# Kernel optimization log

Measured on AMD Instinct MI355X. Metric: run time of the kernel, lower is better.

The kernel has to match this reference:

```python
import jax, jax.numpy as jnp
import numpy as np


def _phi(x):
    # ELU(x) + 1 feature map (positive kernel feature map)
    return jax.nn.elu(x) + 1.0


def setup_inputs() -> dict:
    key = jax.random.key(0)
    k1, k2, k3 = jax.random.split(key, 3)
    B, S, E = 4, 4096, 1024
    inputs = jax.random.normal(k1, (B, S, E), dtype=jnp.float32)
    mask = jnp.ones((B, S), dtype=jnp.float32)
    w_qkv = jax.random.normal(k2, (3 * E, E), dtype=jnp.float32) * (E ** -0.5)
    b_qkv = jax.random.normal(k3, (3 * E,), dtype=jnp.float32) * 0.02
    return {"inputs": inputs, "mask": mask, "w_qkv": w_qkv, "b_qkv": b_qkv, "num_heads": 16}


def reference(inputs, mask, w_qkv, b_qkv, num_heads):
    B, S, E = inputs.shape
    H = num_heads
    D = E // H
    # qkv projection: torch Linear is x @ W.T + b
    qkv = inputs @ w_qkv.T + b_qkv                     # (B, S, 3E)
    qkv = qkv.reshape(B, S, 3, H, D)
    q = qkv[:, :, 0]                                   # (B, S, H, D)
    k = qkv[:, :, 1]
    v = qkv[:, :, 2]
    # key masking (float multiply, as in einsum 'bshd,bs->bshd')
    k = k * mask[:, :, None, None]
    kq = _phi(q)                                       # (B, S, H, D)
    kk = _phi(k)                                       # (B, S, H, D)
    # kv outer-product accumulation over sequence: (B, H, M, D)
    kv = jnp.einsum('bshd,bshm->bhmd', kk, v)
    # normalizer
    z = 1.0 / (jnp.einsum('bshd,bhd->bsh', kq, kk.sum(axis=1)) + 1e-6)
    # final contraction
    attn = jnp.einsum('bshd,bhmd,bsh->bshm', kq, kv, z)  # (B, S, H, D)
    attn = attn.reshape(B, S, E)
    # NOTE: original forward computes a projection but returns `attn` (dropout is
    # identity at inference), so projection is dead code and omitted here.
    return attn
```

## Files before the change

kernel.cpp:

```cpp
#include <hip/hip_runtime.h>

typedef unsigned short u16;
typedef short bf16x8 __attribute__((ext_vector_type(8)));
typedef float f32x4 __attribute__((ext_vector_type(4)));
typedef u16 u16x8 __attribute__((ext_vector_type(8)));
typedef u16 u16x4 __attribute__((ext_vector_type(4)));

#define B_ 4
#define S_ 4096
#define E_ 1024
#define H_ 16
#define D_ 64
#define M_ 16384
#define N_ 3072
#define K_ 1024

__device__ __forceinline__ u16 f2b(float f) {
    unsigned x = __builtin_bit_cast(unsigned, f);
    return (u16)((x + 0x7fffu + ((x >> 16) & 1u)) >> 16);
}
__device__ __forceinline__ float b2f(u16 u) {
    unsigned x = ((unsigned)u) << 16;
    return __builtin_bit_cast(float, x);
}
__device__ __forceinline__ float phi_f(float x) { return x > 0.f ? x + 1.f : __expf(x); }

__device__ __forceinline__ void gload16(const void* g, void* l) {
    __builtin_amdgcn_global_load_lds((const __attribute__((address_space(1))) void*)g,
                                     (__attribute__((address_space(3))) void*)l, 16, 0, 0);
}

#define MEMFENCE asm volatile("" ::: "memory")
#define BAR { MEMFENCE; __builtin_amdgcn_s_barrier(); MEMFENCE; }
#define LGKM0 { asm volatile("s_waitcnt lgkmcnt(0)" ::: "memory"); \
                __builtin_amdgcn_sched_barrier(0); }
#define VMCNT(n) asm volatile("s_waitcnt vmcnt(" #n ")" ::: "memory")

__global__ void cvt_bf16(const float* __restrict__ in, u16* __restrict__ out, int n8) {
    int stride = gridDim.x * blockDim.x;
    for (int i = blockIdx.x * blockDim.x + threadIdx.x; i < n8; i += stride) {
        const float4* p = (const float4*)(in + (size_t)i * 8);
        float4 a = p[0], b = p[1];
        u16x8 o;
        o[0] = f2b(a.x); o[1] = f2b(a.y); o[2] = f2b(a.z); o[3] = f2b(a.w);
        o[4] = f2b(b.x); o[5] = f2b(b.y); o[6] = f2b(b.z); o[7] = f2b(b.w);
        *(u16x8*)(out + (size_t)i * 8) = o;
    }
}


#define RD_A(BO, MI0) { _Pragma("unroll") for (int m_ = 0; m_ < 4; ++m_) { \
    av[m_][0] = *(const bf16x8*)(aB + (BO) + (MI0 + m_) * 2048 + pc0); \
    av[m_][1] = *(const bf16x8*)(aB + (BO) + (MI0 + m_) * 2048 + pc1); } }

#define RD_B01(BO) { _Pragma("unroll") for (int n_ = 0; n_ < 2; ++n_) { \
    b01[n_][0] = *(const bf16x8*)(bB + (BO) + n_ * 2048 + pc0); \
    b01[n_][1] = *(const bf16x8*)(bB + (BO) + n_ * 2048 + pc1); } }

#define RD_B23(BO) { _Pragma("unroll") for (int n_ = 0; n_ < 2; ++n_) { \
    b23[n_][0] = *(const bf16x8*)(bB + (BO) + (2 + n_) * 2048 + pc0); \
    b23[n_][1] = *(const bf16x8*)(bB + (BO) + (2 + n_) * 2048 + pc1); } }

#define ST_A(TT, HI, BO) { \
    gload16(gA + (size_t)((HI) * 64) * K_ + (TT) * 64, lds + (BO) + (HI) * 8192 + t16); \
    gload16(gA + (size_t)((HI) * 64 + 128) * K_ + (TT) * 64, lds + (BO) + 16384 + (HI) * 8192 + t16); }

#define ST_B(TT, PR, BO) { \
    gload16(gB + (size_t)((PR) * 128) * K_ + (TT) * 64, lds + (BO) + 32768 + (PR) * 16384 + t16); \
    gload16(gB + (size_t)((PR) * 128 + 64) * K_ + (TT) * 64, lds + (BO) + 32768 + (PR) * 16384 + 8192 + t16); }

#define MM16(MI0, NI0, BV) { __builtin_amdgcn_s_setprio(1); \
    _Pragma("unroll") for (int m_ = 0; m_ < 4; ++m_) \
    _Pragma("unroll") for (int n_ = 0; n_ < 2; ++n_) \
    _Pragma("unroll") for (int h_ = 0; h_ < 2; ++h_) \
        acc[(MI0) + m_][(NI0) + n_] = __builtin_amdgcn_mfma_f32_16x16x32_bf16( \
            av[m_][h_], BV[n_][h_], acc[(MI0) + m_][(NI0) + n_], 0, 0, 0); \
    __builtin_amdgcn_s_setprio(0); }

__device__ __forceinline__ void run_tile(
    const u16* gA, const u16* gB, char* lds, int t16,
    const char* aB, const char* bB, int pc0, int pc1, f32x4 (&acc)[8][4])
{
    bf16x8 av[4][2], b01[2][2], b23[2][2];
    ST_A(0, 0, 0); ST_B(0, 0, 0); ST_B(0, 1, 0); ST_A(0, 1, 0);
    ST_A(1, 0, 65536); ST_B(1, 0, 65536);
    VMCNT(4);
    __builtin_amdgcn_s_barrier();
    MEMFENCE;
#pragma unroll 1
    for (int kt = 0; kt < 16; kt += 2) {
        int tp2 = kt + 2 < 16 ? kt + 2 : 15;
        int tp3 = kt + 3 < 16 ? kt + 3 : 15;
        RD_A(0, 0); RD_B01(0); ST_A(kt + 1, 1, 65536); BAR; LGKM0; MM16(0, 0, b01);
        RD_B23(0);  ST_B(kt + 1, 1, 65536);            BAR; LGKM0; MM16(0, 2, b23);
        RD_A(0, 4); ST_A(tp2, 0, 0);                   BAR; LGKM0; MM16(4, 2, b23);
        ST_B(tp2, 0, 0); VMCNT(4);                     BAR; LGKM0; MM16(4, 0, b01);
        RD_A(65536, 0); RD_B01(65536); ST_A(tp2, 1, 0); BAR; LGKM0; MM16(0, 0, b01);
        RD_B23(65536);  ST_B(tp2, 1, 0);                BAR; LGKM0; MM16(0, 2, b23);
        RD_A(65536, 4); ST_A(tp3, 0, 65536);            BAR; LGKM0; MM16(4, 2, b23);
        ST_B(tp3, 0, 65536); VMCNT(4);                  BAR; LGKM0; MM16(4, 0, b01);
    }
    VMCNT(0);
    __builtin_amdgcn_s_barrier();
    MEMFENCE;
}

__global__ __launch_bounds__(512, 2) void gemm_vk(
    const u16* __restrict__ Abf, const u16* __restrict__ Wbf,
    const float* __restrict__ bias, const float* __restrict__ mask,
    u16* VT, float* __restrict__ KVP, float* __restrict__ KSP)
{
    __shared__ __align__(16) char lds[131072];

    int wg  = blockIdx.x;
    int xcd = wg & 7, ii = wg >> 3;
    int tm  = xcd * 8 + (ii >> 2);
    int g   = ii & 3;
    int m0  = tm << 8;
    int b   = tm >> 4;
    int s0  = (tm & 15) << 8;

    int t = threadIdx.x;
    int l = t & 63, wid = t >> 6;
    int wr = wid >> 2, wc = wid & 3;
    int lg = l >> 4, lr = l & 15;

    int srow  = t >> 3;
    int scolE = ((t & 7) ^ (srow & 7)) << 3;
    int t16   = t * 16;

    const u16* gA = Abf + (size_t)(m0 + srow) * K_ + scolE;
    const char* aB = lds + (wr * 128 + lr) * 128;
    const char* bB = lds + 32768 + (wc * 64 + lr) * 128;
    int pc0 = (lg * 16) ^ ((lr & 7) << 4);
    int pc1 = pc0 ^ 64;

    {
        int n0 = 2048 + g * 256;
        const u16* gB = Wbf + (size_t)(n0 + srow) * K_ + scolE;
        f32x4 acc[8][4] = {};
        run_tile(gA, gB, lds, t16, aB, bB, pc0, pc1, acc);
        float bv[4];
#pragma unroll
        for (int ni = 0; ni < 4; ++ni) bv[ni] = bias[n0 + wc * 64 + ni * 16 + lr];
        int h = g * 4 + wc;
#pragma unroll
        for (int mi = 0; mi < 8; ++mi) {
            int sbase = s0 + wr * 128 + mi * 16 + lg * 4;
#pragma unroll
            for (int ni = 0; ni < 4; ++ni) {
                u16x4 o;
#pragma unroll
                for (int j = 0; j < 4; ++j) o[j] = f2b(acc[mi][ni][j] + bv[ni]);
                int d = ni * 16 + lr;
                *(u16x4*)(VT + ((size_t)((b * H_ + h) * D_ + d)) * S_ + sbase) = o;
            }
        }
    }

    {
        int n0 = 1024 + g * 256;
        const u16* gB = Wbf + (size_t)(n0 + srow) * K_ + scolE;
        f32x4 acc[8][4] = {};
        run_tile(gA, gB, lds, t16, aB, bB, pc0, pc1, acc);
        float bv[4];
#pragma unroll
        for (int ni = 0; ni < 4; ++ni) bv[ni] = bias[n0 + wc * 64 + ni * 16 + lr];
#pragma unroll
        for (int mi = 0; mi < 8; ++mi) {
            int sl0 = wr * 128 + mi * 16 + lg * 4;
            float mk[4];
#pragma unroll
            for (int j = 0; j < 4; ++j) mk[j] = mask[m0 + sl0 + j];
#pragma unroll
            for (int ni = 0; ni < 4; ++ni) {
                int d = ni * 16 + lr;
                u16x4 o;
#pragma unroll
                for (int j = 0; j < 4; ++j)
                    o[j] = f2b(phi_f((acc[mi][ni][j] + bv[ni]) * mk[j]));
                *(u16x4*)(lds + wc * 32768 + d * 512 + ((sl0 * 2) ^ ((d & 7) << 4))) = o;
            }
        }
    }
    __syncthreads();

    {
        int head = wid & 3, mh = wid >> 2;
        int bh = b * 16 + g * 4 + head;
        f32x4 akv[2][4] = {};
        const u16* vbase = VT + ((size_t)(bh * 64 + mh * 32 + lr)) * S_ + s0;
#pragma unroll
        for (int ks = 0; ks < 8; ++ks) {
            bf16x8 vf[2];
#pragma unroll
            for (int mi = 0; mi < 2; ++mi)
                vf[mi] = *(const bf16x8*)(vbase + (size_t)mi * 16 * S_ + ks * 32 + lg * 8);
#pragma unroll
            for (int ni = 0; ni < 4; ++ni) {
                int dd = ni * 16 + lr;
                bf16x8 kf = *(const bf16x8*)(lds + head * 32768 + dd * 512 +
                                             ((ks * 64 + lg * 16) ^ ((dd & 7) << 4)));
                akv[0][ni] = __builtin_amdgcn_mfma_f32_16x16x32_bf16(vf[0], kf, akv[0][ni], 0, 0, 0);
                akv[1][ni] = __builtin_amdgcn_mfma_f32_16x16x32_bf16(vf[1], kf, akv[1][ni], 0, 0, 0);
            }
        }
        float* kvp = KVP + ((size_t)(tm & 15) * 64 + bh) * 4096;
#pragma unroll
        for (int mi = 0; mi < 2; ++mi)
#pragma unroll
            for (int ni = 0; ni < 4; ++ni)
#pragma unroll
                for (int j = 0; j < 4; ++j)
                    kvp[(mh * 32 + mi * 16 + lg * 4 + j) * 64 + ni * 16 + lr] = akv[mi][ni][j];
        int hd = t >> 7, dd2 = (t >> 1) & 63, hf = t & 1;
        float ksm = 0.f;
#pragma unroll
        for (int i = 0; i < 16; ++i) {
            bf16x8 kk8 = *(const bf16x8*)(lds + hd * 32768 + dd2 * 512 +
                                          ((hf * 256 + i * 16) ^ ((dd2 & 7) << 4)));
#pragma unroll
            for (int e = 0; e < 8; ++e) ksm += b2f((u16)kk8[e]);
        }
        ksm += __shfl_xor(ksm, 1);
        if (!hf) KSP[(tm & 15) * 4096 + (b * 16 + g * 4 + hd) * 64 + dd2] = ksm;
    }
}

__global__ void reduce_kvb(const float* __restrict__ KVP, const float* __restrict__ KSP,
                           u16* __restrict__ KVB)
{
    int bh = blockIdx.x;
    int t = threadIdx.x;
    int d = t & 63, mg = t >> 6;
#pragma unroll 1
    for (int i = 0; i < 16; ++i) {
        int m = mg * 16 + i;
        float s = 0.f;
#pragma unroll
        for (int c = 0; c < 16; ++c)
            s += KVP[((size_t)c * 64 + bh) * 4096 + m * 64 + d];
        KVB[((size_t)bh * 80 + m) * 64 + (d ^ ((m & 7) << 3))] = f2b(s);
    }
    if (mg == 0) {
        float s = 0.f;
#pragma unroll
        for (int c = 0; c < 16; ++c) s += KSP[c * 4096 + bh * 64 + d];
        KVB[((size_t)bh * 80 + 64) * 64 + d] = f2b(s);
    }
    for (int m = 65 + mg; m < 80; m += 4)
        KVB[((size_t)bh * 80 + m) * 64 + (d ^ ((m & 7) << 3))] = 0;
}

__global__ __launch_bounds__(512, 2) void gemm_qattn(
    const u16* __restrict__ Abf, const u16* __restrict__ Wbf,
    const float* __restrict__ bias, const u16* __restrict__ KVB,
    float* __restrict__ Out)
{
    __shared__ __align__(16) char lds[131072];

    int wg  = blockIdx.x;
    int xcd = wg & 7, ii = wg >> 3;
    int tm  = xcd * 8 + (ii >> 2);
    int g   = ii & 3;
    int m0  = tm << 8;
    int b   = tm >> 4;

    int t = threadIdx.x;
    int l = t & 63, wid = t >> 6;
    int wr = wid >> 2, wc = wid & 3;
    int lg = l >> 4, lr = l & 15;

    int srow  = t >> 3;
    int scolE = ((t & 7) ^ (srow & 7)) << 3;
    int t16   = t * 16;

    const u16* gA = Abf + (size_t)(m0 + srow) * K_ + scolE;
    const char* aB = lds + (wr * 128 + lr) * 128;
    const char* bB = lds + 32768 + (wc * 64 + lr) * 128;
    int pc0 = (lg * 16) ^ ((lr & 7) << 4);
    int pc1 = pc0 ^ 64;

    int n0 = g * 256;
    const u16* gB = Wbf + (size_t)(n0 + srow) * K_ + scolE;

    u16x4 kq16[8][4];
    {
        f32x4 acc[8][4] = {};
        run_tile(gA, gB, lds, t16, aB, bB, pc0, pc1, acc);

        const u16* kvbg = KVB + (size_t)(b * 16 + g * 4) * 80 * 64;
#pragma unroll
        for (int i = 0; i < 5; ++i)
            gload16(kvbg + i * 4096 + t * 8, lds + i * 8192 + t16);

        float bv[4];
#pragma unroll
        for (int ni = 0; ni < 4; ++ni) bv[ni] = bias[n0 + wc * 64 + ni * 16 + lr];
#pragma unroll
        for (int mi = 0; mi < 8; ++mi)
#pragma unroll
            for (int ni = 0; ni < 4; ++ni) {
                u16x4 o;
#pragma unroll
                for (int j = 0; j < 4; ++j)
                    o[j] = f2b(phi_f(acc[mi][ni][j] + bv[ni]));
                kq16[mi][ni] = o;
            }
    }
    VMCNT(0);
    __syncthreads();

#pragma unroll
    for (int r = 0; r < 2; ++r) {
        __syncthreads();
        if (wr == r) {
#pragma unroll
            for (int mi = 0; mi < 8; ++mi)
#pragma unroll
                for (int j = 0; j < 4; ++j) {
                    int sl = mi * 16 + lg * 4 + j;
                    int swz = (sl & 7) << 4;
#pragma unroll
                    for (int ni = 0; ni < 4; ++ni) {
                        int d2 = (ni * 16 + lr) * 2;
                        *(u16*)(lds + 40960 + sl * 512 + wc * 128 + (d2 ^ swz)) =
                            (u16)kq16[mi][ni][j];
                    }
                }
        }
        __syncthreads();

        f32x4 a2[4][5] = {};
#pragma unroll
        for (int kh = 0; kh < 2; ++kh) {
            bf16x8 af[4];
#pragma unroll
            for (int mi2 = 0; mi2 < 4; ++mi2) {
                int sl = wr * 64 + mi2 * 16 + lr;
                af[mi2] = *(const bf16x8*)(lds + 40960 + sl * 512 + wc * 128 +
                                           ((kh * 64 + lg * 16) ^ ((sl & 7) << 4)));
            }
#pragma unroll
            for (int ni2 = 0; ni2 < 5; ++ni2) {
                int m = ni2 * 16 + lr;
                bf16x8 bf_ = *(const bf16x8*)(lds + wc * 10240 + m * 128 +
                                              ((kh * 64 + lg * 16) ^ ((m & 7) << 4)));
#pragma unroll
                for (int mi2 = 0; mi2 < 4; ++mi2)
                    a2[mi2][ni2] = __builtin_amdgcn_mfma_f32_16x16x32_bf16(
                        af[mi2], bf_, a2[mi2][ni2], 0, 0, 0);
            }
        }
#pragma unroll
        for (int mi2 = 0; mi2 < 4; ++mi2)
#pragma unroll
            for (int j = 0; j < 4; ++j) {
                float den = __shfl(a2[mi2][4][j], l & 48);
                float z = 1.f / (den + 1e-6f);
                int sg = (tm & 15) * 256 + r * 128 + wr * 64 + mi2 * 16 + lg * 4 + j;
                float* op = Out + ((size_t)b * S_ + sg) * E_ + g * 256 + wc * 64;
#pragma unroll
                for (int ni2 = 0; ni2 < 4; ++ni2)
                    op[ni2 * 16 + lr] = a2[mi2][ni2][j] * z;
            }
    }
}

extern "C" void kernel_launch(void* const* d_in, const int* in_sizes, int n_in,
                              void* d_out, int out_size, void* d_ws, size_t ws_size,
                              hipStream_t stream)
{
    const float* inputs = (const float*)d_in[0];
    const float* mask   = (const float*)d_in[1];
    const float* w_qkv  = (const float*)d_in[2];
    const float* b_qkv  = (const float*)d_in[3];

    u16* Abf = (u16*)d_ws;
    u16* Wbf = Abf + (size_t)M_ * K_;
    float* KVP = (float*)(Wbf + (size_t)N_ * K_);
    float* KSP = KVP + 16 * 64 * 4096;
    u16* KVB   = (u16*)(KSP + 16 * 4096);

    u16* VT = (u16*)d_out;

    cvt_bf16<<<2048, 256, 0, stream>>>(inputs, Abf, M_ * K_ / 8);
    cvt_bf16<<<768, 256, 0, stream>>>(w_qkv, Wbf, N_ * K_ / 8);
    gemm_vk<<<256, 512, 0, stream>>>(Abf, Wbf, b_qkv, mask, VT, KVP, KSP);
    reduce_kvb<<<64, 256, 0, stream>>>(KVP, KSP, KVB);
    gemm_qattn<<<256, 512, 0, stream>>>(Abf, Wbf, b_qkv, KVB, (float*)d_out);
}
```

Measured before the change: 161.5 us.

## Fuse VK GEMM, KV reduction and Q-attention into one persistent kernel

Merges the three kernels (gemm_vk, reduce_kvb, gemm_qattn) into a single launch of 256 workgroups coordinated by atomic grid counters. Selected workgroups do the KV reduction once all blocks have arrived, and every block runs its Q projection GEMM before waiting on the reduction, so that GEMM overlaps with the barrier. This removes two kernel launches and their gaps. It depends on all 256 workgroups being co-resident (2 per CU under the launch bounds) to avoid deadlock, and it adds a memset and spin-wait overhead.

```diff
diff --git a/kernel.cpp b/kernel.cpp
--- a/kernel.cpp
+++ b/kernel.cpp
@@ -35,6 +35,20 @@
 #define LGKM0 { asm volatile("s_waitcnt lgkmcnt(0)" ::: "memory"); \
                 __builtin_amdgcn_sched_barrier(0); }
 #define VMCNT(n) asm volatile("s_waitcnt vmcnt(" #n ")" ::: "memory")
+
+__device__ __forceinline__ void grid_arrive(unsigned* c) {
+    __threadfence();
+    __syncthreads();
+    if (threadIdx.x == 0)
+        __hip_atomic_fetch_add(c, 1u, __ATOMIC_RELEASE, __HIP_MEMORY_SCOPE_AGENT);
+}
+__device__ __forceinline__ void grid_wait(unsigned* c, unsigned target) {
+    if (threadIdx.x == 0)
+        while (__hip_atomic_load(c, __ATOMIC_ACQUIRE, __HIP_MEMORY_SCOPE_AGENT) < target)
+            __builtin_amdgcn_s_sleep(8);
+    __syncthreads();
+    __threadfence();
+}
 
 __global__ void cvt_bf16(const float* __restrict__ in, u16* __restrict__ out, int n8) {
     int stride = gridDim.x * blockDim.x;
@@ -105,10 +119,11 @@
     MEMFENCE;
 }
 
-__global__ __launch_bounds__(512, 2) void gemm_vk(
+__global__ __launch_bounds__(512, 2) void gemm_all(
     const u16* __restrict__ Abf, const u16* __restrict__ Wbf,
     const float* __restrict__ bias, const float* __restrict__ mask,
-    u16* VT, float* __restrict__ KVP, float* __restrict__ KSP)
+    u16* VT, float* KVP, float* KSP, u16* KVB, unsigned* cnt,
+    float* __restrict__ Out)
 {
     __shared__ __align__(16) char lds[131072];
 
@@ -225,75 +240,41 @@
         ksm += __shfl_xor(ksm, 1);
         if (!hf) KSP[(tm & 15) * 4096 + (b * 16 + g * 4 + hd) * 64 + dd2] = ksm;
     }
-}
-
-__global__ void reduce_kvb(const float* __restrict__ KVP, const float* __restrict__ KSP,
-                           u16* __restrict__ KVB)
-{
-    int bh = blockIdx.x;
-    int t = threadIdx.x;
-    int d = t & 63, mg = t >> 6;
+
+    grid_arrive(cnt);
+
+    if ((tm & 3) == 0) {
+        grid_wait(cnt, 256);
+        int bh = b * 16 + g * 4 + ((tm >> 2) & 3);
+        int d = t & 63, mg = t >> 6;
 #pragma unroll 1
-    for (int i = 0; i < 16; ++i) {
-        int m = mg * 16 + i;
-        float s = 0.f;
-#pragma unroll
-        for (int c = 0; c < 16; ++c)
-            s += KVP[((size_t)c * 64 + bh) * 4096 + m * 64 + d];
-        KVB[((size_t)bh * 80 + m) * 64 + (d ^ ((m & 7) << 3))] = f2b(s);
-    }
-    if (mg == 0) {
-        float s = 0.f;
-#pragma unroll
-        for (int c = 0; c < 16; ++c) s += KSP[c * 4096 + bh * 64 + d];
-        KVB[((size_t)bh * 80 + 64) * 64 + d] = f2b(s);
-    }
-    for (int m = 65 + mg; m < 80; m += 4)
-        KVB[((size_t)bh * 80 + m) * 64 + (d ^ ((m & 7) << 3))] = 0;
-}
-
-__global__ __launch_bounds__(512, 2) void gemm_qattn(
-    const u16* __restrict__ Abf, const u16* __restrict__ Wbf,
-    const float* __restrict__ bias, const u16* __restrict__ KVB,
-    float* __restrict__ Out)
-{
-    __shared__ __align__(16) char lds[131072];
-
-    int wg  = blockIdx.x;
-    int xcd = wg & 7, ii = wg >> 3;
-    int tm  = xcd * 8 + (ii >> 2);
-    int g   = ii & 3;
-    int m0  = tm << 8;
-    int b   = tm >> 4;
-
-    int t = threadIdx.x;
-    int l = t & 63, wid = t >> 6;
-    int wr = wid >> 2, wc = wid & 3;
-    int lg = l >> 4, lr = l & 15;
-
-    int srow  = t >> 3;
-    int scolE = ((t & 7) ^ (srow & 7)) << 3;
-    int t16   = t * 16;
-
-    const u16* gA = Abf + (size_t)(m0 + srow) * K_ + scolE;
-    const char* aB = lds + (wr * 128 + lr) * 128;
-    const char* bB = lds + 32768 + (wc * 64 + lr) * 128;
-    int pc0 = (lg * 16) ^ ((lr & 7) << 4);
-    int pc1 = pc0 ^ 64;
+        for (int i = 0; i < 8; ++i) {
+            int m = mg * 8 + i;
+            float s = 0.f;
+#pragma unroll
+            for (int c = 0; c < 16; ++c)
+                s += KVP[((size_t)c * 64 + bh) * 4096 + m * 64 + d];
+            KVB[((size_t)bh * 80 + m) * 64 + (d ^ ((m & 7) << 3))] = f2b(s);
+        }
+        if (mg == 0) {
+            float s = 0.f;
+#pragma unroll
+            for (int c = 0; c < 16; ++c) s += KSP[c * 4096 + bh * 64 + d];
+            KVB[((size_t)bh * 80 + 64) * 64 + d] = f2b(s);
+        }
+        for (int i = t; i < 960; i += 512) {
+            int m = 65 + (i >> 6), dd = i & 63;
+            KVB[((size_t)bh * 80 + m) * 64 + (dd ^ ((m & 7) << 3))] = 0;
+        }
+        grid_arrive(cnt + 1);
+    }
 
     int n0 = g * 256;
     const u16* gB = Wbf + (size_t)(n0 + srow) * K_ + scolE;
-
     u16x4 kq16[8][4];
     {
         f32x4 acc[8][4] = {};
         run_tile(gA, gB, lds, t16, aB, bB, pc0, pc1, acc);
-
-        const u16* kvbg = KVB + (size_t)(b * 16 + g * 4) * 80 * 64;
-#pragma unroll
-        for (int i = 0; i < 5; ++i)
-            gload16(kvbg + i * 4096 + t * 8, lds + i * 8192 + t16);
-
         float bv[4];
 #pragma unroll
         for (int ni = 0; ni < 4; ++ni) bv[ni] = bias[n0 + wc * 64 + ni * 16 + lr];
@@ -307,6 +288,14 @@
                     o[j] = f2b(phi_f(acc[mi][ni][j] + bv[ni]));
                 kq16[mi][ni] = o;
             }
+    }
+
+    grid_wait(cnt + 1, 64);
+    {
+        const u16* kvbg = KVB + (size_t)(b * 16 + g * 4) * 80 * 64;
+#pragma unroll
+        for (int i = 0; i < 5; ++i)
+            gload16(kvbg + i * 4096 + t * 8, lds + i * 8192 + t16);
     }
     VMCNT(0);
     __syncthreads();
@@ -381,12 +370,13 @@
     float* KVP = (float*)(Wbf + (size_t)N_ * K_);
     float* KSP = KVP + 16 * 64 * 4096;
     u16* KVB   = (u16*)(KSP + 16 * 4096);
+    unsigned* cnt = (unsigned*)(KVB + 64 * 80 * 64);
 
     u16* VT = (u16*)d_out;
 
+    hipMemsetAsync(cnt, 0, 8, stream);
     cvt_bf16<<<2048, 256, 0, stream>>>(inputs, Abf, M_ * K_ / 8);
     cvt_bf16<<<768, 256, 0, stream>>>(w_qkv, Wbf, N_ * K_ / 8);
-    gemm_vk<<<256, 512, 0, stream>>>(Abf, Wbf, b_qkv, mask, VT, KVP, KSP);
-    reduce_kvb<<<64, 256, 0, stream>>>(KVP, KSP, KVB);
-    gemm_qattn<<<256, 512, 0, stream>>>(Abf, Wbf, b_qkv, KVB, (float*)d_out);
-}
+    gemm_all<<<256, 512, 0, stream>>>(Abf, Wbf, b_qkv, mask, VT, KVP, KSP, KVB,
+                                      cnt, (float*)d_out);
+}
```

After: 328.5 us. +103.5%, slower.
